# Optimization experiments

Measured on AMD Instinct MI355X. Metric: run time of the kernel, lower is better.

Reference implementation:

```python
import jax, jax.numpy as jnp
import numpy as np

B, N, D, H = 2, 2048, 1024, 16
DK = D // H


def setup_inputs() -> dict:
    key = jax.random.key(0)
    ks = jax.random.split(key, 8)
    s = 1.0 / np.sqrt(D)  # keep projection outputs O(1)
    return {
        "x": jax.random.normal(ks[0], (B, N, D), jnp.float32),
        "alpha": jax.random.uniform(ks[1], (B, N), jnp.float32, -1.0, 1.0),
        "bias": jax.random.normal(ks[2], (B, N, N), jnp.float32) * 0.1,
        "Wq": jax.random.normal(ks[3], (D, D), jnp.float32) * s,
        "bq": jnp.zeros((D,), jnp.float32),
        "Wk": jax.random.normal(ks[4], (D, D), jnp.float32) * s,
        "bk": jnp.zeros((D,), jnp.float32),
        "Wv": jax.random.normal(ks[5], (D, D), jnp.float32) * s,
        "bv": jnp.zeros((D,), jnp.float32),
        "Wo": jax.random.normal(ks[6], (D, D), jnp.float32) * s,
        "bo": jnp.zeros((D,), jnp.float32),
    }


def reference(x, alpha, bias, Wq, bq, Wk, bk, Wv, bv, Wo, bo):
    b, n, d = x.shape
    # projections -> (B, H, N, DK)
    def split_heads(t):
        return t.reshape(b, n, H, DK).transpose(0, 2, 1, 3)

    q = split_heads(x @ Wq + bq)
    k = split_heads(x @ Wk + bk)
    v = split_heads(x @ Wv + bv)

    # salience rescale of keys/values: (B,1,N,1)
    scale = 1.0 + alpha[:, None, :, None]
    k = k * scale
    v = v * scale

    logits = jnp.einsum("bhnd,bhmd->bhnm", q, k) / np.float32(np.sqrt(DK))
    logits = logits + bias[:, None, :, :]  # broadcast over heads
    attn = jax.nn.softmax(logits, axis=-1)

    y = jnp.einsum("bhnm,bhmd->bhnd", attn, v)
    y = y.transpose(0, 2, 1, 3).reshape(b, n, d)
    return y @ Wo + bo
```

## Files before the change

### kernel.cpp

```cpp
#include <hip/hip_runtime.h>

typedef __attribute__((ext_vector_type(8))) short bf16x8;
typedef __attribute__((ext_vector_type(4))) float f32x4;

#define LOG2E 1.4426950408889634f

static __device__ __forceinline__ unsigned short f2bf(float f) {
    unsigned int u = __builtin_bit_cast(unsigned int, f);
    u += 0x7fffu + ((u >> 16) & 1u);
    return (unsigned short)(u >> 16);
}
static __device__ __forceinline__ void gload_lds16(const void* g, void* l) {
    __builtin_amdgcn_global_load_lds(
        (const __attribute__((address_space(1))) void*)g,
        (__attribute__((address_space(3))) void*)l, 16, 0, 0);
}

__launch_bounds__(256)
__global__ void prep(const float* __restrict__ x,
                     unsigned short* __restrict__ xb,
                     const float* __restrict__ W0, const float* __restrict__ W1,
                     const float* __restrict__ W2, const float* __restrict__ W3,
                     unsigned short* __restrict__ T0, unsigned short* __restrict__ T1,
                     unsigned short* __restrict__ T2, unsigned short* __restrict__ T3) {
    int id = blockIdx.x, tid = threadIdx.x;

    if (id < 2048) {
        int i = id * 256 + tid;
        const float4* s4 = (const float4*)x;
        float4 a = s4[2 * i], b = s4[2 * i + 1];
        uint4 u;
        u.x = (unsigned)f2bf(a.x) | ((unsigned)f2bf(a.y) << 16);
        u.y = (unsigned)f2bf(a.z) | ((unsigned)f2bf(a.w) << 16);
        u.z = (unsigned)f2bf(b.x) | ((unsigned)f2bf(b.y) << 16);
        u.w = (unsigned)f2bf(b.z) | ((unsigned)f2bf(b.w) << 16);
        *(uint4*)(xb + 8 * (size_t)i) = u;
        return;
    }
    {
        __shared__ float t[32][33];
        int j = id - 2048, which = j >> 10, r = j & 1023;
        const float* W = (which == 0) ? W0 : (which == 1) ? W1
                         : (which == 2) ? W2 : W3;
        unsigned short* Wt = (which == 0) ? T0 : (which == 1) ? T1
                             : (which == 2) ? T2 : T3;
        int tx = tid & 31, ty = tid >> 5;
        int x0 = (r & 31) * 32, y0 = (r >> 5) * 32;
        for (int i = 0; i < 4; i++)
            t[ty + 8 * i][tx] = W[(size_t)(y0 + ty + 8 * i) * 1024 + x0 + tx];
        __syncthreads();
        for (int i = 0; i < 4; i++)
            Wt[(size_t)(x0 + ty + 8 * i) * 1024 + y0 + tx] =
                f2bf(t[tx][ty + 8 * i]);
    }
}

__launch_bounds__(256)
__global__ void gemm_qkv(const unsigned short* __restrict__ A,
                         const unsigned short* __restrict__ WqT,
                         const unsigned short* __restrict__ WkT,
                         const unsigned short* __restrict__ WvT,
                         const float* __restrict__ bq,
                         const float* __restrict__ bk,
                         const float* __restrict__ bv,
                         const float* __restrict__ alpha,
                         const float* __restrict__ bias2d,
                         unsigned short* __restrict__ biasP,
                         unsigned short* __restrict__ Qb,
                         unsigned short* __restrict__ Kb,
                         unsigned short* __restrict__ Vtb) {
    __shared__ __align__(16) unsigned short sh[16384];
    int tid = threadIdx.x;

    if (blockIdx.y >= 24) {
        int id = blockIdx.x + 32 * (blockIdx.y - 24);
        int mt = id & 31, qt = (id >> 5) & 15, b = id >> 9;
        const float* s = bias2d + (size_t)b * 2048 * 2048;
        for (int p = 0; p < 8; p++) {
            int row = p * 16 + (tid >> 4), f4 = tid & 15;
            float4 v = *(const float4*)
                &s[(size_t)(qt * 128 + row) * 2048 + mt * 64 + f4 * 4];
            uint2 u;
            u.x = (unsigned)f2bf(v.x * LOG2E) | ((unsigned)f2bf(v.y * LOG2E) << 16);
            u.y = (unsigned)f2bf(v.z * LOG2E) | ((unsigned)f2bf(v.w * LOG2E) << 16);
            *(uint2*)&sh[row * 68 + f4 * 4] = u;
        }
        __syncthreads();
        int w = tid >> 6, lane = tid & 63, quad = lane >> 4, l16 = lane & 15;
        unsigned short* d = biasP + (((size_t)(b * 16 + qt) * 32 + mt) * 8192);
        for (int e = 0; e < 2; e++) {
            unsigned short vals[16];
            for (int c = 0; c < 4; c++)
                for (int rr = 0; rr < 4; rr++)
                    vals[c * 4 + rr] =
                        sh[(e * 64 + w * 16 + quad * 4 + rr) * 68 + c * 16 + l16];
            unsigned short* o = d + ((size_t)((e * 4 + w) * 64 + lane)) * 16;
            *(bf16x8*)&o[0] = *(bf16x8*)&vals[0];
            *(bf16x8*)&o[8] = *(bf16x8*)&vals[8];
        }
        return;
    }

    unsigned short (*As)[64] = (unsigned short(*)[64])sh;
    unsigned short (*Bs)[64] = (unsigned short(*)[64])(sh + 8192);
    int which = blockIdx.y >> 3;
    const unsigned short* Bt = (which == 0) ? WqT : (which == 1) ? WkT : WvT;
    const float* bias = (which == 0) ? bq : (which == 1) ? bk : bv;

    int wave = tid >> 6, lane = tid & 63, quad = lane >> 4, l16 = lane & 15;
    int wm = wave & 1, wn = wave >> 1;
    int lrow = lane >> 3, lblk = lane & 7;
    int swz = ((lblk ^ lrow) * 8);
    int m0 = blockIdx.x * 128, n0 = (blockIdx.y & 7) * 128;
    f32x4 acc[4][4] = {};

    for (int kt = 0; kt < 16; kt++) {
        int k0 = kt * 64;
        for (int i = 0; i < 4; i++) {
            int rbase = i * 32 + wave * 8;
            gload_lds16(&A[(size_t)(m0 + rbase + lrow) * 1024 + k0 + swz],
                        &As[rbase][0]);
            gload_lds16(&Bt[(size_t)(n0 + rbase + lrow) * 1024 + k0 + swz],
                        &Bs[rbase][0]);
        }
        __syncthreads();
        for (int ks = 0; ks < 2; ks++) {
            int pblk = ((ks * 4 + quad) ^ (l16 & 7)) * 8;
            bf16x8 af[4], bf_[4];
            for (int i = 0; i < 4; i++)
                af[i] = *(const bf16x8*)&As[64 * wm + 16 * i + l16][pblk];
            for (int j = 0; j < 4; j++)
                bf_[j] = *(const bf16x8*)&Bs[64 * wn + 16 * j + l16][pblk];
            if (which == 2) {
                for (int i = 0; i < 4; i++)
                    for (int j = 0; j < 4; j++)
                        acc[i][j] = __builtin_amdgcn_mfma_f32_16x16x32_bf16(
                            af[i], bf_[j], acc[i][j], 0, 0, 0);
            } else {
                for (int i = 0; i < 4; i++)
                    for (int j = 0; j < 4; j++)
                        acc[i][j] = __builtin_amdgcn_mfma_f32_16x16x32_bf16(
                            bf_[j], af[i], acc[i][j], 0, 0, 0);
            }
        }
        __syncthreads();
    }

    if (which == 2) {
        for (int i = 0; i < 4; i++)
            for (int j = 0; j < 4; j++) {
                int colb = n0 + 64 * wn + 16 * j + l16;
                int h = colb >> 6, dk = colb & 63;
                int row0 = m0 + 64 * wm + 16 * i + quad * 4;
                int bb = row0 >> 11, nn0 = row0 & 2047;
                unsigned short v4[4];
                for (int r = 0; r < 4; r++) {
                    float v = acc[i][j][r] + bias[colb];
                    v4[r] = f2bf(v * (1.0f + alpha[bb * 2048 + nn0 + r]));
                }
                uint2 u;
                u.x = (unsigned)v4[0] | ((unsigned)v4[1] << 16);
                u.y = (unsigned)v4[2] | ((unsigned)v4[3] << 16);
                *(uint2*)&Vtb[((size_t)(bb * 16 + h) * 64 + dk) * 2048 + nn0] = u;
            }
    } else {
        unsigned short* outb = (which == 0) ? Qb : Kb;
        for (int i = 0; i < 4; i++)
            for (int j = 0; j < 4; j++) {
                int row = m0 + 64 * wm + 16 * i + l16;
                int bb = row >> 11, nn = row & 2047;
                int colb0 = n0 + 64 * wn + 16 * j + quad * 4;
                int h = colb0 >> 6, dk0 = colb0 & 63;
                float4 b4 = *(const float4*)&bias[colb0];
                float s = (which == 0) ? (0.125f * LOG2E)
                                       : (1.0f + alpha[bb * 2048 + nn]);
                unsigned short v4[4];
                v4[0] = f2bf((acc[i][j][0] + b4.x) * s);
                v4[1] = f2bf((acc[i][j][1] + b4.y) * s);
                v4[2] = f2bf((acc[i][j][2] + b4.z) * s);
                v4[3] = f2bf((acc[i][j][3] + b4.w) * s);
                uint2 u;
                u.x = (unsigned)v4[0] | ((unsigned)v4[1] << 16);
                u.y = (unsigned)v4[2] | ((unsigned)v4[3] << 16);
                *(uint2*)&outb[((size_t)(bb * 16 + h) * 2048 + nn) * 64 + dk0] = u;
            }
    }
}

__launch_bounds__(256)
__global__ void gemm_out(const unsigned short* __restrict__ A,
                         const unsigned short* __restrict__ Bt,
                         const float* __restrict__ bias,
                         float* __restrict__ outf) {
    __shared__ __align__(16) unsigned short As[128][64];
    __shared__ __align__(16) unsigned short Bs[64][64];
    int tid = threadIdx.x;
    int wave = tid >> 6, lane = tid & 63, quad = lane >> 4, l16 = lane & 15;
    int wm = wave & 1, wn = wave >> 1;
    int lrow = lane >> 3, lblk = lane & 7;
    int swz = ((lblk ^ lrow) * 8);
    int m0 = blockIdx.x * 128, n0 = blockIdx.y * 64;
    f32x4 acc[4][2] = {};

    for (int kt = 0; kt < 16; kt++) {
        int k0 = kt * 64;
        for (int i = 0; i < 4; i++) {
            int rbase = i * 32 + wave * 8;
            gload_lds16(&A[(size_t)(m0 + rbase + lrow) * 1024 + k0 + swz],
                        &As[rbase][0]);
        }
        for (int i = 0; i < 2; i++) {
            int rbase = i * 32 + wave * 8;
            gload_lds16(&Bt[(size_t)(n0 + rbase + lrow) * 1024 + k0 + swz],
                        &Bs[rbase][0]);
        }
        __syncthreads();
        for (int ks = 0; ks < 2; ks++) {
            int pblk = ((ks * 4 + quad) ^ (l16 & 7)) * 8;
            bf16x8 af[4], bf_[2];
            for (int i = 0; i < 4; i++)
                af[i] = *(const bf16x8*)&As[64 * wm + 16 * i + l16][pblk];
            for (int j = 0; j < 2; j++)
                bf_[j] = *(const bf16x8*)&Bs[32 * wn + 16 * j + l16][pblk];
            for (int i = 0; i < 4; i++)
                for (int j = 0; j < 2; j++)
                    acc[i][j] = __builtin_amdgcn_mfma_f32_16x16x32_bf16(
                        bf_[j], af[i], acc[i][j], 0, 0, 0);
        }
        __syncthreads();
    }

    for (int i = 0; i < 4; i++)
        for (int j = 0; j < 2; j++) {
            int row = m0 + 64 * wm + 16 * i + l16;
            int colb0 = n0 + 32 * wn + 16 * j + quad * 4;
            float4 b4 = *(const float4*)&bias[colb0];
            float4 o;
            o.x = acc[i][j][0] + b4.x;
            o.y = acc[i][j][1] + b4.y;
            o.z = acc[i][j][2] + b4.z;
            o.w = acc[i][j][3] + b4.w;
            *(float4*)&outf[(size_t)row * 1024 + colb0] = o;
        }
}

__launch_bounds__(256, 4)
__global__ void attn_kernel(const unsigned short* __restrict__ Q,
                            const unsigned short* __restrict__ K,
                            const unsigned short* __restrict__ Vt,
                            const unsigned short* __restrict__ biasP,
                            unsigned short* __restrict__ Y,
                            float* __restrict__ Opart,
                            float* __restrict__ Lpart, int split) {
    __shared__ __align__(16) unsigned short Ks[64][64];
    __shared__ __align__(16) unsigned short Vs[64][64];
    __shared__ __align__(16) unsigned short Ps[4][32][72];
    int tid = threadIdx.x;
    int wave = tid >> 6, lane = tid & 63, quad = lane >> 4, l16 = lane & 15;
    int qt = blockIdx.x, h = blockIdx.y;
    int b, mt0, mtN;
    if (split) { b = blockIdx.z >> 1; int half = blockIdx.z & 1;
                 mt0 = half * 16; mtN = mt0 + 16; }
    else       { b = blockIdx.z; mt0 = 0; mtN = 32; }
    int q0 = qt * 128;
    size_t headoff = (size_t)(b * 16 + h) * 2048 * 64;
    const unsigned short* Kp = K + headoff;
    const unsigned short* Vp = Vt + headoff;
    int lrow = lane >> 3, lblk = lane & 7;
    int swz = (lblk ^ lrow) * 8;

    bf16x8 aq[2][2];
    for (int e = 0; e < 2; e++) {
        const unsigned short* qp =
            Q + headoff + (size_t)(q0 + e * 64 + wave * 16 + l16) * 64;
        aq[e][0] = *(const bf16x8*)&qp[quad * 8];
        aq[e][1] = *(const bf16x8*)&qp[32 + quad * 8];
    }
    bf16x8 ones;
    for (int j = 0; j < 8; j++) ones[j] = (short)0x3F80;

    f32x4 oacc[2][4] = {};
    f32x4 lacc[2] = {};
    const unsigned short* bP = biasP + (size_t)(b * 16 + qt) * 32 * 8192;

    for (int mt = mt0; mt < mtN; mt++) {
        int m0 = mt * 64;
        for (int i = 0; i < 2; i++) {
            int rbase = wave * 16 + i * 8;
            gload_lds16(&Kp[(size_t)(m0 + rbase + lrow) * 64 + swz], &Ks[rbase][0]);
            gload_lds16(&Vp[(size_t)(rbase + lrow) * 2048 + m0 + swz], &Vs[rbase][0]);
        }
        const unsigned short* bt = bP + (size_t)mt * 8192;
        bf16x8 bz[2][2];
        for (int e = 0; e < 2; e++) {
            const unsigned short* p = bt + (size_t)((e * 4 + wave) * 64 + lane) * 16;
            bz[e][0] = *(const bf16x8*)&p[0];
            bz[e][1] = *(const bf16x8*)&p[8];
        }
        __syncthreads();

        f32x4 sc[2][4];
        for (int e = 0; e < 2; e++)
            for (int c = 0; c < 4; c++) {
                uint2 w = ((const uint2*)&bz[e][c >> 1])[c & 1];
                f32x4 s;
                s[0] = __builtin_bit_cast(float, w.x << 16);
                s[1] = __builtin_bit_cast(float, w.x & 0xffff0000u);
                s[2] = __builtin_bit_cast(float, w.y << 16);
                s[3] = __builtin_bit_cast(float, w.y & 0xffff0000u);
                sc[e][c] = s;
            }
        __builtin_amdgcn_s_setprio(1);
        for (int c = 0; c < 4; c++) {
            for (int ks = 0; ks < 2; ks++) {
                bf16x8 kf = *(const bf16x8*)&Ks[c * 16 + l16]
                                               [((ks * 4 + quad) ^ (l16 & 7)) * 8];
                sc[0][c] = __builtin_amdgcn_mfma_f32_16x16x32_bf16(aq[0][ks], kf, sc[0][c], 0, 0, 0);
                sc[1][c] = __builtin_amdgcn_mfma_f32_16x16x32_bf16(aq[1][ks], kf, sc[1][c], 0, 0, 0);
            }
        }
        __builtin_amdgcn_s_setprio(0);

        for (int e = 0; e < 2; e++)
            for (int c = 0; c < 4; c++) {
                int colw = (((c * 2 + (l16 >> 3)) + quad) & 7) * 8 + (l16 & 7);
                for (int r = 0; r < 4; r++) {
                    float p = exp2f(sc[e][c][r]);
                    unsigned int u = __builtin_bit_cast(unsigned int, p);
                    Ps[wave][e * 16 + quad * 4 + r][colw] = (unsigned short)(u >> 16);
                }
            }

        __builtin_amdgcn_s_setprio(1);
        for (int ks = 0; ks < 2; ks++) {
            int blkr = (ks * 4 + quad + (l16 >> 2)) & 7;
            bf16x8 pf0 = *(const bf16x8*)&Ps[wave][l16][blkr * 8];
            bf16x8 pf1 = *(const bf16x8*)&Ps[wave][16 + l16][blkr * 8];
            lacc[0] = __builtin_amdgcn_mfma_f32_16x16x32_bf16(pf0, ones, lacc[0], 0, 0, 0);
            lacc[1] = __builtin_amdgcn_mfma_f32_16x16x32_bf16(pf1, ones, lacc[1], 0, 0, 0);
            for (int cv = 0; cv < 4; cv++) {
                bf16x8 vf = *(const bf16x8*)&Vs[cv * 16 + l16]
                                               [((ks * 4 + quad) ^ (l16 & 7)) * 8];
                oacc[0][cv] = __builtin_amdgcn_mfma_f32_16x16x32_bf16(pf0, vf, oacc[0][cv], 0, 0, 0);
                oacc[1][cv] = __builtin_amdgcn_mfma_f32_16x16x32_bf16(pf1, vf, oacc[1][cv], 0, 0, 0);
            }
        }
        __builtin_amdgcn_s_setprio(0);
        __syncthreads();
    }

    if (split) {
        size_t p = ((size_t)((b * 16 + h) * 16 + qt)) * 2 + (blockIdx.z & 1);
        float* Op = Opart + p * 8192;
        for (int e = 0; e < 2; e++)
            for (int cv = 0; cv < 4; cv++)
                for (int r = 0; r < 4; r++)
                    Op[(e * 64 + wave * 16 + quad * 4 + r) * 64 + cv * 16 + l16] =
                        oacc[e][cv][r];
        if (l16 == 0)
            for (int e = 0; e < 2; e++)
                for (int r = 0; r < 4; r++)
                    Lpart[p * 128 + e * 64 + wave * 16 + quad * 4 + r] = lacc[e][r];
    } else {
        for (int e = 0; e < 2; e++) {
            float invl[4];
            for (int r = 0; r < 4; r++) invl[r] = 1.0f / lacc[e][r];
            for (int cv = 0; cv < 4; cv++)
                for (int r = 0; r < 4; r++) {
                    int qrow = q0 + e * 64 + 16 * wave + quad * 4 + r;
                    int d = h * 64 + cv * 16 + l16;
                    Y[((size_t)b * 2048 + qrow) * 1024 + d] =
                        f2bf(oacc[e][cv][r] * invl[r]);
                }
        }
    }
}

__global__ void attn_combine(const float* __restrict__ Opart,
                             const float* __restrict__ Lpart,
                             unsigned short* __restrict__ Y) {
    int blk = blockIdx.x;
    int qt = blk & 15, h = (blk >> 4) & 15, b = blk >> 8;
    const float* O0 = Opart + (size_t)blk * 2 * 8192;
    const float* O1 = O0 + 8192;
    const float* L0 = Lpart + (size_t)blk * 2 * 128;
    const float* L1 = L0 + 128;
    int t = threadIdx.x;
    for (int i = 0; i < 8; i++) {
        int idx4 = i * 256 + t;
        int q = idx4 >> 4;
        int dk = (idx4 & 15) * 4;
        float4 a = *(const float4*)&O0[idx4 * 4];
        float4 c = *(const float4*)&O1[idx4 * 4];
        float inv = 1.0f / (L0[q] + L1[q]);
        uint2 u;
        u.x = (unsigned)f2bf((a.x + c.x) * inv) |
              ((unsigned)f2bf((a.y + c.y) * inv) << 16);
        u.y = (unsigned)f2bf((a.z + c.z) * inv) |
              ((unsigned)f2bf((a.w + c.w) * inv) << 16);
        int qrow = qt * 128 + q;
        *(uint2*)&Y[((size_t)b * 2048 + qrow) * 1024 + h * 64 + dk] = u;
    }
}

extern "C" void kernel_launch(void* const* d_in, const int* in_sizes, int n_in,
                              void* d_out, int out_size, void* d_ws, size_t ws_size,
                              hipStream_t stream) {
    const float* x     = (const float*)d_in[0];
    const float* alpha = (const float*)d_in[1];
    const float* bias  = (const float*)d_in[2];
    const float* Wq    = (const float*)d_in[3];
    const float* bq    = (const float*)d_in[4];
    const float* Wk    = (const float*)d_in[5];
    const float* bk    = (const float*)d_in[6];
    const float* Wv    = (const float*)d_in[7];
    const float* bv    = (const float*)d_in[8];
    const float* Wo    = (const float*)d_in[9];
    const float* bo    = (const float*)d_in[10];
    float* out = (float*)d_out;

    char* ws = (char*)d_ws;
    const size_t MB = 1048576;
    unsigned short* xb    = (unsigned short*)(ws);
    unsigned short* wqt   = (unsigned short*)(ws + 8 * MB);
    unsigned short* wkt   = (unsigned short*)(ws + 10 * MB);
    unsigned short* wvt   = (unsigned short*)(ws + 12 * MB);
    unsigned short* wot   = (unsigned short*)(ws + 14 * MB);
    unsigned short* Qb    = (unsigned short*)(ws + 16 * MB);
    unsigned short* Kb    = (unsigned short*)(ws + 24 * MB);
    unsigned short* Vtb   = (unsigned short*)(ws + 32 * MB);
    unsigned short* biasP = (unsigned short*)(ws + 40 * MB);
    float*          Opart = (float*)(ws + 56 * MB);
    float*          Lpart = (float*)(ws + 88 * MB);
    unsigned short* Yb    = xb;
    int split = (ws_size >= 90 * MB) ? 1 : 0;

    prep<<<6144, 256, 0, stream>>>(x, xb, Wq, Wk, Wv, Wo, wqt, wkt, wvt, wot);

    gemm_qkv<<<dim3(32, 56), 256, 0, stream>>>(
        xb, wqt, wkt, wvt, bq, bk, bv, alpha, bias, biasP, Qb, Kb, Vtb);

    if (split) {
        attn_kernel<<<dim3(16, 16, 4), 256, 0, stream>>>(
            Qb, Kb, Vtb, biasP, Yb, Opart, Lpart, 1);
        attn_combine<<<512, 256, 0, stream>>>(Opart, Lpart, Yb);
    } else {
        attn_kernel<<<dim3(16, 16, 2), 256, 0, stream>>>(
            Qb, Kb, Vtb, biasP, Yb, Opart, Lpart, 0);
    }

    gemm_out<<<dim3(32, 16), 256, 0, stream>>>(Yb, wot, bo, out);
}
```

Before: 235.7 us.

## Replace split-KV attention plus combine with 64-row query tiles over full KV

The attention kernel no longer splits the key range in two and merges the halves with a separate combine kernel. Each block now handles 64 query rows instead of 128 over all 32 key tiles, so the grid still has 1024 blocks and each block normalises and writes its output directly. The grid is reordered with heads on the fastest axis so blocks that share a bias tile run close together. This removes the fp32 partial-output traffic and one launch, at the cost of reusing each K/V tile across half as many query rows, which doubles K/V load traffic per query.

```diff
diff --git a/kernel.cpp b/kernel.cpp
--- a/kernel.cpp
+++ b/kernel.cpp
@@ -249,41 +249,36 @@
                             const unsigned short* __restrict__ K,
                             const unsigned short* __restrict__ Vt,
                             const unsigned short* __restrict__ biasP,
-                            unsigned short* __restrict__ Y,
-                            float* __restrict__ Opart,
-                            float* __restrict__ Lpart, int split) {
+                            unsigned short* __restrict__ Y) {
     __shared__ __align__(16) unsigned short Ks[64][64];
     __shared__ __align__(16) unsigned short Vs[64][64];
-    __shared__ __align__(16) unsigned short Ps[4][32][72];
+    __shared__ __align__(16) unsigned short Ps[4][16][72];
     int tid = threadIdx.x;
     int wave = tid >> 6, lane = tid & 63, quad = lane >> 4, l16 = lane & 15;
-    int qt = blockIdx.x, h = blockIdx.y;
-    int b, mt0, mtN;
-    if (split) { b = blockIdx.z >> 1; int half = blockIdx.z & 1;
-                 mt0 = half * 16; mtN = mt0 + 16; }
-    else       { b = blockIdx.z; mt0 = 0; mtN = 32; }
-    int q0 = qt * 128;
+    int h = blockIdx.x, qt = blockIdx.y, b = blockIdx.z;
+    int q0 = qt * 64;
+    int eh = qt & 1;
     size_t headoff = (size_t)(b * 16 + h) * 2048 * 64;
     const unsigned short* Kp = K + headoff;
     const unsigned short* Vp = Vt + headoff;
     int lrow = lane >> 3, lblk = lane & 7;
     int swz = (lblk ^ lrow) * 8;
 
-    bf16x8 aq[2][2];
-    for (int e = 0; e < 2; e++) {
+    bf16x8 aq[2];
+    {
         const unsigned short* qp =
-            Q + headoff + (size_t)(q0 + e * 64 + wave * 16 + l16) * 64;
-        aq[e][0] = *(const bf16x8*)&qp[quad * 8];
-        aq[e][1] = *(const bf16x8*)&qp[32 + quad * 8];
+            Q + headoff + (size_t)(q0 + wave * 16 + l16) * 64;
+        aq[0] = *(const bf16x8*)&qp[quad * 8];
+        aq[1] = *(const bf16x8*)&qp[32 + quad * 8];
     }
     bf16x8 ones;
     for (int j = 0; j < 8; j++) ones[j] = (short)0x3F80;
 
-    f32x4 oacc[2][4] = {};
-    f32x4 lacc[2] = {};
-    const unsigned short* bP = biasP + (size_t)(b * 16 + qt) * 32 * 8192;
-
-    for (int mt = mt0; mt < mtN; mt++) {
+    f32x4 oacc[4] = {};
+    f32x4 lacc = {};
+    const unsigned short* bP = biasP + (size_t)(b * 16 + (qt >> 1)) * 32 * 8192;
+
+    for (int mt = 0; mt < 32; mt++) {
         int m0 = mt * 64;
         for (int i = 0; i < 2; i++) {
             int rbase = wave * 16 + i * 8;
@@ -291,116 +286,69 @@
             gload_lds16(&Vp[(size_t)(rbase + lrow) * 2048 + m0 + swz], &Vs[rbase][0]);
         }
         const unsigned short* bt = bP + (size_t)mt * 8192;
-        bf16x8 bz[2][2];
-        for (int e = 0; e < 2; e++) {
-            const unsigned short* p = bt + (size_t)((e * 4 + wave) * 64 + lane) * 16;
-            bz[e][0] = *(const bf16x8*)&p[0];
-            bz[e][1] = *(const bf16x8*)&p[8];
-        }
-        __syncthreads();
-
-        f32x4 sc[2][4];
-        for (int e = 0; e < 2; e++)
-            for (int c = 0; c < 4; c++) {
-                uint2 w = ((const uint2*)&bz[e][c >> 1])[c & 1];
-                f32x4 s;
-                s[0] = __builtin_bit_cast(float, w.x << 16);
-                s[1] = __builtin_bit_cast(float, w.x & 0xffff0000u);
-                s[2] = __builtin_bit_cast(float, w.y << 16);
-                s[3] = __builtin_bit_cast(float, w.y & 0xffff0000u);
-                sc[e][c] = s;
-            }
+        bf16x8 bz[2];
+        {
+            const unsigned short* p =
+                bt + (size_t)((eh * 4 + wave) * 64 + lane) * 16;
+            bz[0] = *(const bf16x8*)&p[0];
+            bz[1] = *(const bf16x8*)&p[8];
+        }
+        __syncthreads();
+
+        f32x4 sc[4];
+        for (int c = 0; c < 4; c++) {
+            uint2 w = ((const uint2*)&bz[c >> 1])[c & 1];
+            f32x4 s;
+            s[0] = __builtin_bit_cast(float, w.x << 16);
+            s[1] = __builtin_bit_cast(float, w.x & 0xffff0000u);
+            s[2] = __builtin_bit_cast(float, w.y << 16);
+            s[3] = __builtin_bit_cast(float, w.y & 0xffff0000u);
+            sc[c] = s;
+        }
         __builtin_amdgcn_s_setprio(1);
         for (int c = 0; c < 4; c++) {
             for (int ks = 0; ks < 2; ks++) {
                 bf16x8 kf = *(const bf16x8*)&Ks[c * 16 + l16]
                                                [((ks * 4 + quad) ^ (l16 & 7)) * 8];
-                sc[0][c] = __builtin_amdgcn_mfma_f32_16x16x32_bf16(aq[0][ks], kf, sc[0][c], 0, 0, 0);
-                sc[1][c] = __builtin_amdgcn_mfma_f32_16x16x32_bf16(aq[1][ks], kf, sc[1][c], 0, 0, 0);
+                sc[c] = __builtin_amdgcn_mfma_f32_16x16x32_bf16(
+                    aq[ks], kf, sc[c], 0, 0, 0);
             }
         }
         __builtin_amdgcn_s_setprio(0);
 
-        for (int e = 0; e < 2; e++)
-            for (int c = 0; c < 4; c++) {
-                int colw = (((c * 2 + (l16 >> 3)) + quad) & 7) * 8 + (l16 & 7);
-                for (int r = 0; r < 4; r++) {
-                    float p = exp2f(sc[e][c][r]);
-                    unsigned int u = __builtin_bit_cast(unsigned int, p);
-                    Ps[wave][e * 16 + quad * 4 + r][colw] = (unsigned short)(u >> 16);
-                }
-            }
+        for (int c = 0; c < 4; c++) {
+            int colw = (((c * 2 + (l16 >> 3)) + quad) & 7) * 8 + (l16 & 7);
+            for (int r = 0; r < 4; r++) {
+                float p = exp2f(sc[c][r]);
+                unsigned int u = __builtin_bit_cast(unsigned int, p);
+                Ps[wave][quad * 4 + r][colw] = (unsigned short)(u >> 16);
+            }
+        }
 
         __builtin_amdgcn_s_setprio(1);
         for (int ks = 0; ks < 2; ks++) {
             int blkr = (ks * 4 + quad + (l16 >> 2)) & 7;
             bf16x8 pf0 = *(const bf16x8*)&Ps[wave][l16][blkr * 8];
-            bf16x8 pf1 = *(const bf16x8*)&Ps[wave][16 + l16][blkr * 8];
-            lacc[0] = __builtin_amdgcn_mfma_f32_16x16x32_bf16(pf0, ones, lacc[0], 0, 0, 0);
-            lacc[1] = __builtin_amdgcn_mfma_f32_16x16x32_bf16(pf1, ones, lacc[1], 0, 0, 0);
+            lacc = __builtin_amdgcn_mfma_f32_16x16x32_bf16(pf0, ones, lacc, 0, 0, 0);
             for (int cv = 0; cv < 4; cv++) {
                 bf16x8 vf = *(const bf16x8*)&Vs[cv * 16 + l16]
                                                [((ks * 4 + quad) ^ (l16 & 7)) * 8];
-                oacc[0][cv] = __builtin_amdgcn_mfma_f32_16x16x32_bf16(pf0, vf, oacc[0][cv], 0, 0, 0);
-                oacc[1][cv] = __builtin_amdgcn_mfma_f32_16x16x32_bf16(pf1, vf, oacc[1][cv], 0, 0, 0);
+                oacc[cv] = __builtin_amdgcn_mfma_f32_16x16x32_bf16(
+                    pf0, vf, oacc[cv], 0, 0, 0);
             }
         }
         __builtin_amdgcn_s_setprio(0);
         __syncthreads();
     }
 
-    if (split) {
-        size_t p = ((size_t)((b * 16 + h) * 16 + qt)) * 2 + (blockIdx.z & 1);
-        float* Op = Opart + p * 8192;
-        for (int e = 0; e < 2; e++)
-            for (int cv = 0; cv < 4; cv++)
-                for (int r = 0; r < 4; r++)
-                    Op[(e * 64 + wave * 16 + quad * 4 + r) * 64 + cv * 16 + l16] =
-                        oacc[e][cv][r];
-        if (l16 == 0)
-            for (int e = 0; e < 2; e++)
-                for (int r = 0; r < 4; r++)
-                    Lpart[p * 128 + e * 64 + wave * 16 + quad * 4 + r] = lacc[e][r];
-    } else {
-        for (int e = 0; e < 2; e++) {
-            float invl[4];
-            for (int r = 0; r < 4; r++) invl[r] = 1.0f / lacc[e][r];
-            for (int cv = 0; cv < 4; cv++)
-                for (int r = 0; r < 4; r++) {
-                    int qrow = q0 + e * 64 + 16 * wave + quad * 4 + r;
-                    int d = h * 64 + cv * 16 + l16;
-                    Y[((size_t)b * 2048 + qrow) * 1024 + d] =
-                        f2bf(oacc[e][cv][r] * invl[r]);
-                }
-        }
-    }
-}
-
-__global__ void attn_combine(const float* __restrict__ Opart,
-                             const float* __restrict__ Lpart,
-                             unsigned short* __restrict__ Y) {
-    int blk = blockIdx.x;
-    int qt = blk & 15, h = (blk >> 4) & 15, b = blk >> 8;
-    const float* O0 = Opart + (size_t)blk * 2 * 8192;
-    const float* O1 = O0 + 8192;
-    const float* L0 = Lpart + (size_t)blk * 2 * 128;
-    const float* L1 = L0 + 128;
-    int t = threadIdx.x;
-    for (int i = 0; i < 8; i++) {
-        int idx4 = i * 256 + t;
-        int q = idx4 >> 4;
-        int dk = (idx4 & 15) * 4;
-        float4 a = *(const float4*)&O0[idx4 * 4];
-        float4 c = *(const float4*)&O1[idx4 * 4];
-        float inv = 1.0f / (L0[q] + L1[q]);
-        uint2 u;
-        u.x = (unsigned)f2bf((a.x + c.x) * inv) |
-              ((unsigned)f2bf((a.y + c.y) * inv) << 16);
-        u.y = (unsigned)f2bf((a.z + c.z) * inv) |
-              ((unsigned)f2bf((a.w + c.w) * inv) << 16);
-        int qrow = qt * 128 + q;
-        *(uint2*)&Y[((size_t)b * 2048 + qrow) * 1024 + h * 64 + dk] = u;
-    }
+    float invl[4];
+    for (int r = 0; r < 4; r++) invl[r] = 1.0f / lacc[r];
+    for (int cv = 0; cv < 4; cv++)
+        for (int r = 0; r < 4; r++) {
+            int qrow = q0 + 16 * wave + quad * 4 + r;
+            int d = h * 64 + cv * 16 + l16;
+            Y[((size_t)b * 2048 + qrow) * 1024 + d] = f2bf(oacc[cv][r] * invl[r]);
+        }
 }
 
 extern "C" void kernel_launch(void* const* d_in, const int* in_sizes, int n_in,
@@ -430,24 +378,15 @@
     unsigned short* Kb    = (unsigned short*)(ws + 24 * MB);
     unsigned short* Vtb   = (unsigned short*)(ws + 32 * MB);
     unsigned short* biasP = (unsigned short*)(ws + 40 * MB);
-    float*          Opart = (float*)(ws + 56 * MB);
-    float*          Lpart = (float*)(ws + 88 * MB);
     unsigned short* Yb    = xb;
-    int split = (ws_size >= 90 * MB) ? 1 : 0;
 
     prep<<<6144, 256, 0, stream>>>(x, xb, Wq, Wk, Wv, Wo, wqt, wkt, wvt, wot);
 
     gemm_qkv<<<dim3(32, 56), 256, 0, stream>>>(
         xb, wqt, wkt, wvt, bq, bk, bv, alpha, bias, biasP, Qb, Kb, Vtb);
 
-    if (split) {
-        attn_kernel<<<dim3(16, 16, 4), 256, 0, stream>>>(
-            Qb, Kb, Vtb, biasP, Yb, Opart, Lpart, 1);
-        attn_combine<<<512, 256, 0, stream>>>(Opart, Lpart, Yb);
-    } else {
-        attn_kernel<<<dim3(16, 16, 2), 256, 0, stream>>>(
-            Qb, Kb, Vtb, biasP, Yb, Opart, Lpart, 0);
-    }
+    attn_kernel<<<dim3(16, 32, 2), 256, 0, stream>>>(
+        Qb, Kb, Vtb, biasP, Yb);
 
     gemm_out<<<dim3(32, 16), 256, 0, stream>>>(Yb, wot, bo, out);
 }
```

New measurement: 238.3 us. Within noise of the previous version (+1.1%).

## Process query sub-tiles sequentially in attention to cut registers and raise occupancy

Applied to the files above, without the earlier changes.

The attention inner loop now handles the two 16-row query sub-tiles one after another instead of interleaved, so only one set of score accumulators is live at a time and the per-wave P staging buffer in LDS is halved. The launch bound is raised from 4 to 6 blocks per CU to use the lower register and LDS footprint. The cost is less independent MFMA work per phase, which means fewer instructions to hide MFMA latency within a wave, and reuse of K/V fragment loads across the two sub-tiles is lost (K/V LDS reads happen twice).

```diff
diff --git a/kernel.cpp b/kernel.cpp
--- a/kernel.cpp
+++ b/kernel.cpp
@@ -244,7 +244,7 @@
         }
 }
 
-__launch_bounds__(256, 4)
+__launch_bounds__(256, 6)
 __global__ void attn_kernel(const unsigned short* __restrict__ Q,
                             const unsigned short* __restrict__ K,
                             const unsigned short* __restrict__ Vt,
@@ -254,7 +254,7 @@
                             float* __restrict__ Lpart, int split) {
     __shared__ __align__(16) unsigned short Ks[64][64];
     __shared__ __align__(16) unsigned short Vs[64][64];
-    __shared__ __align__(16) unsigned short Ps[4][32][72];
+    __shared__ __align__(16) unsigned short Ps[4][16][72];
     int tid = threadIdx.x;
     int wave = tid >> 6, lane = tid & 63, quad = lane >> 4, l16 = lane & 15;
     int qt = blockIdx.x, h = blockIdx.y;
@@ -299,53 +299,50 @@
         }
         __syncthreads();
 
-        f32x4 sc[2][4];
-        for (int e = 0; e < 2; e++)
+        for (int e = 0; e < 2; e++) {
+            f32x4 sc[4];
             for (int c = 0; c < 4; c++) {
                 uint2 w = ((const uint2*)&bz[e][c >> 1])[c & 1];
-                f32x4 s;
-                s[0] = __builtin_bit_cast(float, w.x << 16);
-                s[1] = __builtin_bit_cast(float, w.x & 0xffff0000u);
-                s[2] = __builtin_bit_cast(float, w.y << 16);
-                s[3] = __builtin_bit_cast(float, w.y & 0xffff0000u);
-                sc[e][c] = s;
-            }
-        __builtin_amdgcn_s_setprio(1);
-        for (int c = 0; c < 4; c++) {
-            for (int ks = 0; ks < 2; ks++) {
-                bf16x8 kf = *(const bf16x8*)&Ks[c * 16 + l16]
-                                               [((ks * 4 + quad) ^ (l16 & 7)) * 8];
-                sc[0][c] = __builtin_amdgcn_mfma_f32_16x16x32_bf16(aq[0][ks], kf, sc[0][c], 0, 0, 0);
-                sc[1][c] = __builtin_amdgcn_mfma_f32_16x16x32_bf16(aq[1][ks], kf, sc[1][c], 0, 0, 0);
-            }
-        }
-        __builtin_amdgcn_s_setprio(0);
-
-        for (int e = 0; e < 2; e++)
+                sc[c][0] = __builtin_bit_cast(float, w.x << 16);
+                sc[c][1] = __builtin_bit_cast(float, w.x & 0xffff0000u);
+                sc[c][2] = __builtin_bit_cast(float, w.y << 16);
+                sc[c][3] = __builtin_bit_cast(float, w.y & 0xffff0000u);
+            }
+            __builtin_amdgcn_s_setprio(1);
+            for (int c = 0; c < 4; c++) {
+                for (int ks = 0; ks < 2; ks++) {
+                    bf16x8 kf = *(const bf16x8*)&Ks[c * 16 + l16]
+                                                   [((ks * 4 + quad) ^ (l16 & 7)) * 8];
+                    sc[c] = __builtin_amdgcn_mfma_f32_16x16x32_bf16(
+                        aq[e][ks], kf, sc[c], 0, 0, 0);
+                }
+            }
+            __builtin_amdgcn_s_setprio(0);
+
             for (int c = 0; c < 4; c++) {
                 int colw = (((c * 2 + (l16 >> 3)) + quad) & 7) * 8 + (l16 & 7);
                 for (int r = 0; r < 4; r++) {
-                    float p = exp2f(sc[e][c][r]);
+                    float p = exp2f(sc[c][r]);
                     unsigned int u = __builtin_bit_cast(unsigned int, p);
-                    Ps[wave][e * 16 + quad * 4 + r][colw] = (unsigned short)(u >> 16);
+                    Ps[wave][quad * 4 + r][colw] = (unsigned short)(u >> 16);
                 }
             }
 
-        __builtin_amdgcn_s_setprio(1);
-        for (int ks = 0; ks < 2; ks++) {
-            int blkr = (ks * 4 + quad + (l16 >> 2)) & 7;
-            bf16x8 pf0 = *(const bf16x8*)&Ps[wave][l16][blkr * 8];
-            bf16x8 pf1 = *(const bf16x8*)&Ps[wave][16 + l16][blkr * 8];
-            lacc[0] = __builtin_amdgcn_mfma_f32_16x16x32_bf16(pf0, ones, lacc[0], 0, 0, 0);
-            lacc[1] = __builtin_amdgcn_mfma_f32_16x16x32_bf16(pf1, ones, lacc[1], 0, 0, 0);
-            for (int cv = 0; cv < 4; cv++) {
-                bf16x8 vf = *(const bf16x8*)&Vs[cv * 16 + l16]
-                                               [((ks * 4 + quad) ^ (l16 & 7)) * 8];
-                oacc[0][cv] = __builtin_amdgcn_mfma_f32_16x16x32_bf16(pf0, vf, oacc[0][cv], 0, 0, 0);
-                oacc[1][cv] = __builtin_amdgcn_mfma_f32_16x16x32_bf16(pf1, vf, oacc[1][cv], 0, 0, 0);
-            }
-        }
-        __builtin_amdgcn_s_setprio(0);
+            __builtin_amdgcn_s_setprio(1);
+            for (int ks = 0; ks < 2; ks++) {
+                int blkr = (ks * 4 + quad + (l16 >> 2)) & 7;
+                bf16x8 pf = *(const bf16x8*)&Ps[wave][l16][blkr * 8];
+                lacc[e] = __builtin_amdgcn_mfma_f32_16x16x32_bf16(
+                    pf, ones, lacc[e], 0, 0, 0);
+                for (int cv = 0; cv < 4; cv++) {
+                    bf16x8 vf = *(const bf16x8*)&Vs[cv * 16 + l16]
+                                                   [((ks * 4 + quad) ^ (l16 & 7)) * 8];
+                    oacc[e][cv] = __builtin_amdgcn_mfma_f32_16x16x32_bf16(
+                        pf, vf, oacc[e][cv], 0, 0, 0);
+                }
+            }
+            __builtin_amdgcn_s_setprio(0);
+        }
         __syncthreads();
     }
 
```

New measurement: 375.8 us. 1.59x slower.
